# Performance work log

Hardware: AMD Instinct MI355X
Metric: run time of the kernel (lower is better)

## Reference

```python
import jax, jax.numpy as jnp
import numpy as np

N = 1_000_000
E = 1_000_000
K = 512
H = 64
F_IN = 19
N_ITERS = 3
EPS = 1e-5

def _leaky(x):
    return jax.nn.leaky_relu(x, negative_slope=0.01)

def _layernorm(x, g, b):
    mu = jnp.mean(x, axis=-1, keepdims=True)
    var = jnp.var(x, axis=-1, keepdims=True)
    return (x - mu) * jax.lax.rsqrt(var + EPS) * g + b

def setup_inputs() -> dict:
    key = jax.random.key(0)
    ks = jax.random.split(key, 20)
    s = 0.1
    inp = {
        "x": jax.random.normal(ks[0], (N, F_IN), dtype=jnp.float32),
        "edge_index": jax.random.randint(ks[1], (2, E), 0, N, dtype=jnp.int64),
        "candidate_indices": jax.random.randint(ks[2], (K,), 0, N, dtype=jnp.int64),
        # embedding params
        "pW_in": jax.random.normal(ks[3], (F_IN, H), dtype=jnp.float32) * s,
        "pb_in": jnp.zeros((H,), dtype=jnp.float32),
        "eW": jax.random.normal(ks[4], (2, H, H), dtype=jnp.float32) * s,
        "eb": jnp.zeros((2, H), dtype=jnp.float32),
        "gamma": jnp.ones((2, H), dtype=jnp.float32),
        "beta": jnp.zeros((2, H), dtype=jnp.float32),
        # bottom-up step MLPs (stacked over n_iters)
        "sW1": jax.random.normal(ks[5], (N_ITERS, H, H), dtype=jnp.float32) * s,
        "sb1": jnp.zeros((N_ITERS, H), dtype=jnp.float32),
        "sW2": jax.random.normal(ks[6], (N_ITERS, H, H), dtype=jnp.float32) * s,
        "sb2": jnp.zeros((N_ITERS, H), dtype=jnp.float32),
        # score head
        "hW1": jax.random.normal(ks[7], (H, H), dtype=jnp.float32) * s,
        "hb1": jnp.zeros((H,), dtype=jnp.float32),
        "hW2": jax.random.normal(ks[8], (H, 1), dtype=jnp.float32) * s,
        "hb2": jnp.zeros((1,), dtype=jnp.float32),
    }
    return inp

def reference(x, edge_index, candidate_indices, pW_in, pb_in, eW, eb, gamma, beta,
              sW1, sb1, sW2, sb2, hW1, hb1, hW2, hb2):
    # TreeNodeEmbedding: proj + 2 residual layers with LayerNorm
    h = _leaky(x @ pW_in + pb_in)
    for i in range(2):
        h = _layernorm(h + _leaky(h @ eW[i] + eb[i]), gamma[i], beta[i])
    parent_idx = edge_index[0]
    child_idx = edge_index[1]
    # Bottom-up message passing: scatter-mean over children, tiny MLP update
    for i in range(N_ITERS):
        child_h = h[child_idx]                                   # [E, H] gather
        sum_p = jax.ops.segment_sum(child_h, parent_idx, num_segments=N)  # [N, H]
        cnt = jax.ops.segment_sum(jnp.ones((E,), dtype=h.dtype), parent_idx, num_segments=N)  # [N]
        mean_p = sum_p / jnp.maximum(cnt, 1.0)[:, None]
        mask = (cnt > 0)[:, None]
        delta = _leaky(mean_p @ sW1[i] + sb1[i]) @ sW2[i] + sb2[i]
        h = h + jnp.where(mask, delta, 0.0)
    # Score head on candidates, softmax over k (all candidates real -> full_logits == scores)
    cand_h = h[candidate_indices]                                # [K, H]
    scores = (_leaky(cand_h @ hW1 + hb1) @ hW2 + hb2)[:, 0]      # [K]
    probs = jax.nn.softmax(scores)
    return probs
```

## Files before the change

### kernel.cpp

```cpp
#include <hip/hip_runtime.h>
#include <hip/hip_bf16.h>
#include <math.h>

#define H 64
#define FIN 19
#define EPSLN 1e-5f

#define TB 1024
#define NWV 16
#define NBLK 256

#define OFF_PW   0
#define OFF_PB   1280
#define OFF_EW   1344
#define OFF_EB   9536
#define OFF_G    9664
#define OFF_BT   9792
#define OFF_W1   9920
#define OFF_W2   22208
#define OFF_B1   34496
#define OFF_B2   34688
#define OFF_HW1  34880
#define OFF_HB1  38976
#define OFF_HW2  39040
#define OFF_HB2  39104
#define WTS_TOTAL 39105

__device__ __forceinline__ float leaky(float v) { return v > 0.f ? v : 0.01f * v; }

__device__ __forceinline__ float wsumf(float v) {
#pragma unroll
  for (int off = 32; off > 0; off >>= 1) v += __shfl_xor(v, off, 64);
  return v;
}

template <typename T>
__device__ __forceinline__ void cst(T* p, T v) {
  __hip_atomic_store(p, v, __ATOMIC_RELAXED, __HIP_MEMORY_SCOPE_AGENT);
}
__device__ __forceinline__ int cld(const int* p) {
  return __hip_atomic_load(p, __ATOMIC_RELAXED, __HIP_MEMORY_SCOPE_AGENT);
}

__device__ __forceinline__ void wsync() {
  asm volatile("" ::: "memory");
  __builtin_amdgcn_wave_barrier();
  asm volatile("" ::: "memory");
}

__device__ __forceinline__ bool detect_bf16(const unsigned short* xs) {
  const int lane = threadIdx.x & 63;
  unsigned a = xs[lane], b = xs[64 + lane];
  unsigned ea = (a >> 7) & 0xFFu, ebx = (b >> 7) & 0xFFu;
  return !__any((int)(ea > 140u || ebx > 140u));
}

__device__ __forceinline__ bool detect_i64(const int* w) {
  const int lane = threadIdx.x & 63;
  return __all((int)(w[2 * lane + 1] == 0));
}

__device__ __forceinline__ float ldf(const void* p, size_t i, bool bf) {
  return bf ? __bfloat162float(((const __hip_bfloat16*)p)[i]) : ((const float*)p)[i];
}

struct WT {
  const void* src[14];
  int off[14], len[14], sl[14], rp[14], rs[14], cs[14];
};

__device__ __forceinline__ void prep_one(const WT& T, bool bf, float* wts, int i) {
  int p = 0;
  while (i >= T.off[p] + T.len[p]) ++p;
  const int loc = i - T.off[p];
  float v;
  if (T.rp[p] == 0) {
    v = ldf(T.src[p], loc, bf);
  } else {
    const int s = loc / T.sl[p];
    const int r = loc - s * T.sl[p];
    const int j = r / T.rp[p];
    const int k = r - j * T.rp[p];
    v = (k < T.rs[p])
            ? ldf(T.src[p], (size_t)s * T.rs[p] * T.cs[p] + (size_t)k * T.cs[p] + j, bf)
            : 0.f;
  }
  cst(&wts[i], v);
}

__global__ __launch_bounds__(256) void prep_wts(WT T, const unsigned short* xs,
                                                float* wts, int total) {
  const bool bf = detect_bf16(xs);
  for (int i = blockIdx.x * 256 + threadIdx.x; i < total; i += gridDim.x * 256)
    prep_one(T, bf, wts, i);
}

__device__ float embed_math(const void* x, const float* wts, float* stg, int v,
                            int lane, bool bf) {
  float xv = (lane < FIN) ? ldf(x, (size_t)v * FIN + lane, bf) : 0.f;
  wsync();
  stg[lane] = xv;
  wsync();
  const float* tp = wts + OFF_PW + lane * 20;
  float a0 = wts[OFF_PB + lane], a1 = 0.f, a2 = 0.f, a3 = 0.f;
#pragma unroll
  for (int k = 0; k < 20; k += 4) {
    float4 m = *(const float4*)&stg[k];
    float4 w = *(const float4*)&tp[k];
    a0 += m.x * w.x; a1 += m.y * w.y; a2 += m.z * w.z; a3 += m.w * w.w;
  }
  float h = leaky((a0 + a1) + (a2 + a3));
#pragma unroll
  for (int L = 0; L < 2; ++L) {
    wsync();
    stg[lane] = h;
    wsync();
    const float* tw = wts + OFF_EW + L * 4096 + lane * 64;
    a0 = wts[OFF_EB + L * 64 + lane]; a1 = a2 = a3 = 0.f;
#pragma unroll
    for (int k = 0; k < H; k += 4) {
      float4 m = *(const float4*)&stg[k];
      float4 w = *(const float4*)&tw[k];
      a0 += m.x * w.x; a1 += m.y * w.y; a2 += m.z * w.z; a3 += m.w * w.w;
    }
    float val = h + leaky((a0 + a1) + (a2 + a3));
    float mu = wsumf(val) * (1.f / 64.f);
    float d = val - mu;
    float var = wsumf(d * d) * (1.f / 64.f);
    h = d * (1.f / sqrtf(var + EPSLN)) * wts[OFF_G + L * 64 + lane] +
        wts[OFF_BT + L * 64 + lane];
  }
  return h;
}

__device__ float delta_math(const float* wts, float* stg, float mean, int it, int lane) {
  wsync();
  stg[lane] = mean;
  wsync();
  const float* w1 = wts + OFF_W1 + it * 4096 + lane * 64;
  float a0 = wts[OFF_B1 + it * 64 + lane], a1 = 0.f, a2 = 0.f, a3 = 0.f;
#pragma unroll
  for (int k = 0; k < H; k += 4) {
    float4 m = *(const float4*)&stg[k];
    float4 w = *(const float4*)&w1[k];
    a0 += m.x * w.x; a1 += m.y * w.y; a2 += m.z * w.z; a3 += m.w * w.w;
  }
  float t1 = leaky((a0 + a1) + (a2 + a3));
  wsync();
  stg[lane] = t1;
  wsync();
  const float* w2 = wts + OFF_W2 + it * 4096 + lane * 64;
  a0 = wts[OFF_B2 + it * 64 + lane]; a1 = a2 = a3 = 0.f;
#pragma unroll
  for (int k = 0; k < H; k += 4) {
    float4 m = *(const float4*)&stg[k];
    float4 w = *(const float4*)&w2[k];
    a0 += m.x * w.x; a1 += m.y * w.y; a2 += m.z * w.z; a3 += m.w * w.w;
  }
  wsync();
  return (a0 + a1) + (a2 + a3);
}

__device__ float score_math(const float* wts, float* stg, float hv, int lane) {
  wsync();
  stg[lane] = hv;
  wsync();
  const float* hw1 = wts + OFF_HW1 + lane * 64;
  float a0 = wts[OFF_HB1 + lane], a1 = 0.f, a2 = 0.f, a3 = 0.f;
#pragma unroll
  for (int k = 0; k < H; k += 4) {
    float4 m = *(const float4*)&stg[k];
    float4 w = *(const float4*)&hw1[k];
    a0 += m.x * w.x; a1 += m.y * w.y; a2 += m.z * w.z; a3 += m.w * w.w;
  }
  wsync();
  float t1 = leaky((a0 + a1) + (a2 + a3));
  return wsumf(t1 * wts[OFF_HW2 + lane]) + wts[OFF_HB2];
}

__global__ __launch_bounds__(256) void init_kernel(int* map, int nN, int* counters, int K,
                                                   int* ch3, int n3, int* ch2, int n2,
                                                   int* ch1, int n1) {
  const int tid = blockIdx.x * 256 + threadIdx.x;
  const int stride = gridDim.x * 256;
  for (int i = tid; i < nN; i += stride) map[i] = 0;
  for (int i = tid; i < n3; i += stride) ch3[i] = -1;
  for (int i = tid; i < n2; i += stride) ch2[i] = -1;
  for (int i = tid; i < n1; i += stride) ch1[i] = -1;
  if (tid < 3) counters[tid] = 0;
  if (tid == 3) counters[3] = K;
}

__global__ __launch_bounds__(64) void seed_kernel(const int* cand_raw, int K, int nN,
                                                  int* map, int* node3, int* nextSame3,
                                                  int* selfChild3, int* ctr2, int cap2,
                                                  int* node2) {
  const bool i64 = detect_i64(cand_raw);
  int t = blockIdx.x * 64 + threadIdx.x;
  if (t >= K) return;
  int cv = i64 ? cand_raw[2 * t] : cand_raw[t];
  unsigned n = (unsigned)cv;
  if (n >= (unsigned)nN) n = 0;
  node3[t] = (int)n;
  int enc = (1 << 24) | t;
  int old = atomicExch(&map[n], enc);
  nextSame3[t] = ((old >> 24) == 1) ? (old & 0xFFFFFF) : -1;
  int s = atomicAdd(ctr2, 1);
  if (s < cap2) { node2[s] = (int)n; selfChild3[t] = s; } else selfChild3[t] = 0;
}

__global__ __launch_bounds__(256) void regself_kernel(const int* ctrU_, int capU,
                                                      const int* nodeU, int* map, int epoch,
                                                      int* nextSameU, int* ctrD, int capD,
                                                      int* nodeD, int* selfChildU) {
  int cnt = *ctrU_; if (cnt > capU) cnt = capU;
  int t = blockIdx.x * 256 + threadIdx.x;
  if (t >= cnt) return;
  int n = nodeU[t];
  int enc = (epoch << 24) | t;
  int old = atomicExch(&map[n], enc);
  nextSameU[t] = ((old >> 24) == epoch) ? (old & 0xFFFFFF) : -1;
  int s = atomicAdd(ctrD, 1);
  if (s < capD) { nodeD[s] = n; selfChildU[t] = s; } else selfChildU[t] = 0;
}

__global__ __launch_bounds__(256) void scan_kernel(const int* eraw, int E, int nN,
                                                   const int* map, int epoch,
                                                   const int* nextSameU, int* childHeadU,
                                                   int* ctrD, int capD, int* nodeD,
                                                   int* childNextD) {
  const bool i64 = detect_i64(eraw);
  int e = blockIdx.x * 256 + threadIdx.x;
  if (e >= E) return;
  int pv = i64 ? eraw[2 * e] : eraw[e];
  unsigned p = (unsigned)pv;
  if (p >= (unsigned)nN) p = 0;
  int m = map[p];
  if ((m >> 24) != epoch) return;
  int cv = i64 ? eraw[2 * (E + e)] : eraw[E + e];
  unsigned c = (unsigned)cv;
  if (c >= (unsigned)nN) c = 0;
  int t = m & 0xFFFFFF;
  while (t >= 0) {
    int ct = atomicAdd(ctrD, 1);
    if (ct < capD) {
      nodeD[ct] = (int)c;
      childNextD[ct] = atomicExch(&childHeadU[t], ct);
    }
    t = nextSameU[t];
  }
}

__global__ __launch_bounds__(64) void eval0_kernel(const void* x, const int* ctr0_,
                                                   int cap0, const int* node0,
                                                   const float* wts, float* val0) {
  __shared__ float stg[H];
  int cnt = *ctr0_; if (cnt > cap0) cnt = cap0;
  const int t = blockIdx.x;
  if (t >= cnt) return;
  const int lane = threadIdx.x;
  const bool bf = detect_bf16((const unsigned short*)x);
  float h = embed_math(x, wts, stg, node0[t], lane, bf);
  val0[(size_t)t * H + lane] = h;
}

__global__ __launch_bounds__(64) void evalL_kernel(const int* ctrU_, int capU,
                                                   const int* selfChildU,
                                                   const int* childHeadU,
                                                   const int* childNextD,
                                                   const float* valD, float* valU,
                                                   const float* wts, int it) {
  __shared__ float stg[H];
  int cnt = *ctrU_; if (cnt > capU) cnt = capU;
  const int t = blockIdx.x;
  if (t >= cnt) return;
  const int lane = threadIdx.x;
  float hv = valD[(size_t)selfChildU[t] * H + lane];
  float acc = 0.f;
  int k = 0;
  int c = childHeadU[t];
  while (c >= 0) { acc += valD[(size_t)c * H + lane]; ++k; c = childNextD[c]; }
  if (k > 0) hv += delta_math(wts, stg, acc / (float)k, it, lane);
  valU[(size_t)t * H + lane] = hv;
}

__global__ __launch_bounds__(512) void score_kernel(
    const float* __restrict__ candH, const float* __restrict__ wts,
    const void* x, void* out, int K) {
  __shared__ float red[512];
  const int t = threadIdx.x;
  const bool bf = detect_bf16((const unsigned short*)x);
  float sc = 0.f;
  if (t < K) {
    float hr[H];
#pragma unroll
    for (int k = 0; k < H; k += 4) {
      float4 v = *(const float4*)&candH[(size_t)t * H + k];
      hr[k] = v.x; hr[k + 1] = v.y; hr[k + 2] = v.z; hr[k + 3] = v.w;
    }
    for (int j = 0; j < H; ++j) {
      float a = wts[OFF_HB1 + j];
#pragma unroll
      for (int k = 0; k < H; k += 4) {
        float4 w = *(const float4*)&wts[OFF_HW1 + j * 64 + k];
        a += hr[k] * w.x + hr[k + 1] * w.y + hr[k + 2] * w.z + hr[k + 3] * w.w;
      }
      sc += leaky(a) * wts[OFF_HW2 + j];
    }
    sc += wts[OFF_HB2];
  }
  red[t] = (t < K) ? sc : -3.0e38f;
  __syncthreads();
  for (int off = 256; off > 0; off >>= 1) {
    if (t < off) red[t] = fmaxf(red[t], red[t + off]);
    __syncthreads();
  }
  const float m = red[0];
  __syncthreads();
  const float ex = (t < K) ? expf(sc - m) : 0.f;
  red[t] = ex;
  __syncthreads();
  for (int off = 256; off > 0; off >>= 1) {
    if (t < off) red[t] += red[t + off];
    __syncthreads();
  }
  const float inv = 1.f / red[0];
  if (t < K) {
    float p = ex * inv;
    if (bf) ((__hip_bfloat16*)out)[t] = __float2bfloat16(p);
    else    ((float*)out)[t] = p;
  }
}

struct FA {
  const void* x; const void* edge; const void* cand; void* outp;
  int nN, E, K, CAP2, CAP1, CAP0;
  int *ctrl;
  int *map3, *map2, *map1;
  int *chHead3, *chHead2, *chHead1;
  float* wts;
  int *nextSame3, *selfCh3;
  int *nextSame2, *selfCh2, *chNext2;
  int *nextSame1, *selfCh1, *chNext1;
  int *node0, *chNext0;
  float *val0, *val1, *val2, *scores;
  WT T;
};

#define CLINE 32

__device__ __forceinline__ void gsync(int* ctrl, int& phase) {
  __syncthreads();
  if (threadIdx.x == 0) {
    ++phase;
    const int nB = (int)gridDim.x;
    const int clu = (int)blockIdx.x >> 5;
    const int nClu = (nB + 31) >> 5;
    int cluSize = nB - (clu << 5);
    if (cluSize > 32) cluSize = 32;
    asm volatile("" ::: "memory");
    int old = __hip_atomic_fetch_add(&ctrl[clu * CLINE], 1, __ATOMIC_RELAXED,
                                     __HIP_MEMORY_SCOPE_AGENT);
    if (old == phase * cluSize - 1) {
      int mold = __hip_atomic_fetch_add(&ctrl[64 * CLINE], 1, __ATOMIC_RELAXED,
                                        __HIP_MEMORY_SCOPE_AGENT);
      if (mold == phase * nClu - 1) {
#pragma unroll
        for (int f = 0; f < 32; ++f)
          __hip_atomic_store(&ctrl[(65 + f) * CLINE], phase, __ATOMIC_RELAXED,
                             __HIP_MEMORY_SCOPE_AGENT);
      }
    }
    int* myFlag = &ctrl[(65 + ((int)blockIdx.x & 31)) * CLINE];
    int guard = 0;
    while (__hip_atomic_load(myFlag, __ATOMIC_RELAXED,
                             __HIP_MEMORY_SCOPE_AGENT) < phase) {
      __builtin_amdgcn_s_sleep(2);
      if (++guard > (1 << 18)) break;
    }
    asm volatile("" ::: "memory");
  }
  __syncthreads();
}

__global__ __launch_bounds__(TB, 4) void fused_kernel(FA A) {
  __shared__ float smem[NWV * H];
  const int tid = threadIdx.x;
  const int lane = tid & 63;
  const int wib = tid >> 6;
  const int gtid = blockIdx.x * TB + tid;
  const int nthr = (int)gridDim.x * TB;
  const int waveId = blockIdx.x * NWV + wib;
  const int nWaves = (int)gridDim.x * NWV;
  float* stg = &smem[wib * H];
  int* ctrl = A.ctrl;
  int* c2 = &ctrl[97 * CLINE];
  int* c1 = &ctrl[98 * CLINE];
  int* c0 = &ctrl[99 * CLINE];
  int phase = 0;

  const bool bf = detect_bf16((const unsigned short*)A.x);
  const int* eraw = (const int*)A.edge;
  const int* craw = (const int*)A.cand;
  const bool i64e = detect_i64(eraw);
  const bool i64c = detect_i64(craw);

  for (int i = gtid; i < WTS_TOTAL; i += nthr) prep_one(A.T, bf, A.wts, i);
  for (int t = gtid; t < A.K; t += nthr) {
    int cv = i64c ? craw[2 * t] : craw[t];
    unsigned n = (unsigned)cv;
    if (n >= (unsigned)A.nN) n = 0;
    cst(&A.nextSame3[t], atomicExch(&A.map3[(int)n], t));
    int s = atomicAdd(c2, 1);
    if (s < A.CAP2) {
      cst(&A.selfCh3[t], s);
      cst(&A.nextSame2[s], atomicExch(&A.map2[(int)n], s));
      int s1 = atomicAdd(c1, 1);
      if (s1 < A.CAP1) {
        cst(&A.selfCh2[s], s1);
        cst(&A.nextSame1[s1], atomicExch(&A.map1[(int)n], s1));
        int s0 = atomicAdd(c0, 1);
        if (s0 < A.CAP0) { cst(&A.node0[s0], (int)n); cst(&A.selfCh1[s1], s0); }
        else cst(&A.selfCh1[s1], 0);
      } else cst(&A.selfCh2[s], 0);
    } else cst(&A.selfCh3[t], 0);
  }
  gsync(ctrl, phase);

  for (int e = gtid; e < A.E; e += nthr) {
    int pv = i64e ? eraw[2 * e] : eraw[e];
    unsigned p = (unsigned)pv;
    if (p >= (unsigned)A.nN) p = 0;
    int t = A.map3[p];
    if (t < 0) continue;
    int cv = i64e ? eraw[2 * (A.E + e)] : eraw[A.E + e];
    unsigned cn = (unsigned)cv;
    if (cn >= (unsigned)A.nN) cn = 0;
    for (; t >= 0; t = A.nextSame3[t]) {
      int ct = atomicAdd(c2, 1);
      if (ct < A.CAP2) {
        cst(&A.chNext2[ct], atomicExch(&A.chHead3[t], ct));
        cst(&A.nextSame2[ct], atomicExch(&A.map2[(int)cn], ct));
        int s1 = atomicAdd(c1, 1);
        if (s1 < A.CAP1) {
          cst(&A.selfCh2[ct], s1);
          cst(&A.nextSame1[s1], atomicExch(&A.map1[(int)cn], s1));
          int s0 = atomicAdd(c0, 1);
          if (s0 < A.CAP0) { cst(&A.node0[s0], (int)cn); cst(&A.selfCh1[s1], s0); }
          else cst(&A.selfCh1[s1], 0);
        } else cst(&A.selfCh2[ct], 0);
      }
    }
  }
  gsync(ctrl, phase);

  for (int e = gtid; e < A.E; e += nthr) {
    int pv = i64e ? eraw[2 * e] : eraw[e];
    unsigned p = (unsigned)pv;
    if (p >= (unsigned)A.nN) p = 0;
    int t = A.map2[p];
    if (t < 0) continue;
    int cv = i64e ? eraw[2 * (A.E + e)] : eraw[A.E + e];
    unsigned cn = (unsigned)cv;
    if (cn >= (unsigned)A.nN) cn = 0;
    for (; t >= 0; t = A.nextSame2[t]) {
      int ct = atomicAdd(c1, 1);
      if (ct < A.CAP1) {
        cst(&A.chNext1[ct], atomicExch(&A.chHead2[t], ct));
        cst(&A.nextSame1[ct], atomicExch(&A.map1[(int)cn], ct));
        int s0 = atomicAdd(c0, 1);
        if (s0 < A.CAP0) { cst(&A.node0[s0], (int)cn); cst(&A.selfCh1[ct], s0); }
        else cst(&A.selfCh1[ct], 0);
      }
    }
  }
  gsync(ctrl, phase);

  for (int e = gtid; e < A.E; e += nthr) {
    int pv = i64e ? eraw[2 * e] : eraw[e];
    unsigned p = (unsigned)pv;
    if (p >= (unsigned)A.nN) p = 0;
    int t = A.map1[p];
    if (t < 0) continue;
    int cv = i64e ? eraw[2 * (A.E + e)] : eraw[A.E + e];
    unsigned cn = (unsigned)cv;
    if (cn >= (unsigned)A.nN) cn = 0;
    for (; t >= 0; t = A.nextSame1[t]) {
      int ct = atomicAdd(c0, 1);
      if (ct < A.CAP0) {
        cst(&A.node0[ct], (int)cn);
        cst(&A.chNext0[ct], atomicExch(&A.chHead1[t], ct));
      }
    }
  }
  gsync(ctrl, phase);

  {
    int cnt = cld(c0);
    if (cnt > A.CAP0) cnt = A.CAP0;
    for (int t = waveId; t < cnt; t += nWaves) {
      float h = embed_math(A.x, A.wts, stg, A.node0[t], lane, bf);
      cst(&A.val0[(size_t)t * H + lane], h);
    }
  }
  gsync(ctrl, phase);

  {
    int cnt = cld(c1);
    if (cnt > A.CAP1) cnt = A.CAP1;
    for (int t = waveId; t < cnt; t += nWaves) {
      float hv = A.val0[(size_t)A.selfCh1[t] * H + lane];
      float acc = 0.f;
      int kc = 0;
      for (int c = A.chHead1[t]; c >= 0; c = A.chNext0[c]) {
        acc += A.val0[(size_t)c * H + lane];
        ++kc;
      }
      if (kc > 0) hv += delta_math(A.wts, stg, acc / (float)kc, 0, lane);
      cst(&A.val1[(size_t)t * H + lane], hv);
    }
  }
  gsync(ctrl, phase);

  {
    int cnt = cld(c2);
    if (cnt > A.CAP2) cnt = A.CAP2;
    for (int t = waveId; t < cnt; t += nWaves) {
      float hv = A.val1[(size_t)A.selfCh2[t] * H + lane];
      float acc = 0.f;
      int kc = 0;
      for (int c = A.chHead2[t]; c >= 0; c = A.chNext1[c]) {
        acc += A.val1[(size_t)c * H + lane];
        ++kc;
      }
      if (kc > 0) hv += delta_math(A.wts, stg, acc / (float)kc, 1, lane);
      cst(&A.val2[(size_t)t * H + lane], hv);
    }
  }
  gsync(ctrl, phase);

  for (int t = waveId; t < A.K; t += nWaves) {
    float hv = A.val2[(size_t)A.selfCh3[t] * H + lane];
    float acc = 0.f;
    int kc = 0;
    for (int c = A.chHead3[t]; c >= 0; c = A.chNext2[c]) {
      acc += A.val2[(size_t)c * H + lane];
      ++kc;
    }
    if (kc > 0) hv += delta_math(A.wts, stg, acc / (float)kc, 2, lane);
    float sc = score_math(A.wts, stg, hv, lane);
    if (lane == 0) cst(&A.scores[t], sc);
  }
  gsync(ctrl, phase);

  if (blockIdx.x == 0) {
    __shared__ float red[TB];
    float lm = -3.0e38f;
    for (int i = tid; i < A.K; i += TB) lm = fmaxf(lm, A.scores[i]);
    red[tid] = lm;
    __syncthreads();
    for (int off = TB / 2; off > 0; off >>= 1) {
      if (tid < off) red[tid] = fmaxf(red[tid], red[tid + off]);
      __syncthreads();
    }
    const float m = red[0];
    __syncthreads();
    float ls = 0.f;
    for (int i = tid; i < A.K; i += TB) {
      float e = expf(A.scores[i] - m);
      A.scores[i] = e;
      ls += e;
    }
    red[tid] = ls;
    __syncthreads();
    for (int off = TB / 2; off > 0; off >>= 1) {
      if (tid < off) red[tid] += red[tid + off];
      __syncthreads();
    }
    const float inv = 1.f / red[0];
    for (int i = tid; i < A.K; i += TB) {
      float pv = A.scores[i] * inv;
      if (bf) ((__hip_bfloat16*)A.outp)[i] = __float2bfloat16(pv);
      else    ((float*)A.outp)[i] = pv;
    }
  }
}

extern "C" void kernel_launch(void* const* d_in, const int* in_sizes, int n_in,
                              void* d_out, int out_size, void* d_ws, size_t ws_size,
                              hipStream_t stream) {
  const void* x   = d_in[0];
  const int* edge = (const int*)d_in[1];
  const int* cand = (const int*)d_in[2];
  const int nN = in_sizes[0] / FIN;
  const int E  = in_sizes[1] / 2;
  const int K  = in_sizes[2];

  if (K > 2048 || K < 128 || E < 128 || nN < 1) return;

  const int CAP2 = 8 * K, CAP1 = 16 * K, CAP0 = 32 * K;

  auto al = [](size_t b) -> size_t { return (b + 255) & ~(size_t)255; };
  const size_t szW   = (size_t)WTS_TOTAL * sizeof(float);
  const size_t szMap = (size_t)nN * sizeof(int);
  const size_t szK   = (size_t)K * sizeof(int);
  const size_t sz2   = (size_t)CAP2 * sizeof(int);
  const size_t sz1   = (size_t)CAP1 * sizeof(int);
  const size_t sz0   = (size_t)CAP0 * sizeof(int);
  const size_t szV0  = (size_t)CAP0 * H * sizeof(float);
  const size_t szV1  = (size_t)CAP1 * H * sizeof(float);
  const size_t szV2  = (size_t)CAP2 * H * sizeof(float);
  const size_t szV3  = (size_t)K * H * sizeof(float);
  const size_t szCtrl = 16384;

  WT T;
  auto setv = [&](int i, const void* s, int o, int l) {
    T.src[i] = s; T.off[i] = o; T.len[i] = l; T.sl[i] = l;
    T.rp[i] = 0; T.rs[i] = 0; T.cs[i] = 0;
  };
  auto setm = [&](int i, const void* s, int o, int l, int sl, int rpad, int rs, int cs) {
    T.src[i] = s; T.off[i] = o; T.len[i] = l; T.sl[i] = sl;
    T.rp[i] = rpad; T.rs[i] = rs; T.cs[i] = cs;
  };
  setm(0,  d_in[3],  OFF_PW,  1280, 1280, 20, 19, 64);
  setv(1,  d_in[4],  OFF_PB,  64);
  setm(2,  d_in[5],  OFF_EW,  8192, 4096, 64, 64, 64);
  setv(3,  d_in[6],  OFF_EB,  128);
  setv(4,  d_in[7],  OFF_G,   128);
  setv(5,  d_in[8],  OFF_BT,  128);
  setm(6,  d_in[9],  OFF_W1,  12288, 4096, 64, 64, 64);
  setm(7,  d_in[11], OFF_W2,  12288, 4096, 64, 64, 64);
  setv(8,  d_in[10], OFF_B1,  192);
  setv(9,  d_in[12], OFF_B2,  192);
  setm(10, d_in[13], OFF_HW1, 4096, 4096, 64, 64, 64);
  setv(11, d_in[14], OFF_HB1, 64);
  setv(12, d_in[15], OFF_HW2, 64);
  setv(13, d_in[16], OFF_HB2, 1);

  int dev = 0, nCU = 0, maxB = 0;
  bool okq = (hipGetDevice(&dev) == hipSuccess) &&
             (hipDeviceGetAttribute(&nCU, hipDeviceAttributeMultiprocessorCount,
                                    dev) == hipSuccess) &&
             (hipOccupancyMaxActiveBlocksPerMultiprocessor(&maxB, fused_kernel, TB,
                                                           0) == hipSuccess) &&
             nCU >= 8 && maxB >= 1;

  const size_t needF = al(szCtrl) + 3 * al(szMap) + al(szK) + al(sz2) + al(sz1) +
                       al(szW) + 2 * al(szK) + 3 * al(sz2) + 3 * al(sz1) +
                       2 * al(sz0) + al(szV0) + al(szV1) + al(szV2) + al(szK);

  if (okq && ws_size >= needF) {
    char* wsb = (char*)d_ws;
    size_t off = 0;
    auto carve = [&](size_t bytes) -> void* {
      void* p = wsb + off;
      off += (bytes + 255) & ~(size_t)255;
      return p;
    };
    FA A;
    A.x = x; A.edge = edge; A.cand = cand; A.outp = d_out;
    A.nN = nN; A.E = E; A.K = K; A.CAP2 = CAP2; A.CAP1 = CAP1; A.CAP0 = CAP0;
    A.ctrl = (int*)carve(szCtrl);
    char* ffs = wsb + off;
    A.map3 = (int*)carve(szMap);
    A.map2 = (int*)carve(szMap);
    A.map1 = (int*)carve(szMap);
    A.chHead3 = (int*)carve(szK);
    A.chHead2 = (int*)carve(sz2);
    A.chHead1 = (int*)carve(sz1);
    const size_t ffbytes = (size_t)((wsb + off) - ffs);
    A.wts = (float*)carve(szW);
    A.nextSame3 = (int*)carve(szK); A.selfCh3 = (int*)carve(szK);
    A.nextSame2 = (int*)carve(sz2); A.selfCh2 = (int*)carve(sz2);
    A.chNext2 = (int*)carve(sz2);
    A.nextSame1 = (int*)carve(sz1); A.selfCh1 = (int*)carve(sz1);
    A.chNext1 = (int*)carve(sz1);
    A.node0 = (int*)carve(sz0); A.chNext0 = (int*)carve(sz0);
    A.val0 = (float*)carve(szV0); A.val1 = (float*)carve(szV1);
    A.val2 = (float*)carve(szV2);
    A.scores = (float*)carve(szK);
    A.T = T;

    int g = NBLK;
    if (g > nCU * maxB) g = nCU * maxB;
    if (g > 2048) g = 2048;
    if (g >= 8) {
      hipMemsetAsync(A.ctrl, 0, szCtrl, stream);
      hipMemsetAsync(ffs, 0xFF, ffbytes, stream);
      fused_kernel<<<g, TB, 0, stream>>>(A);
      return;
    }
  }

  {
    const size_t need = al(szW) + al(szMap) + 256 +
                        4 * al(szK) + 5 * al(sz2) + 5 * al(sz1) + 2 * al(sz0) +
                        al(szV0) + al(szV1) + al(szV2) + al(szV3);
    if (ws_size < need) return;

    char* wsb = (char*)d_ws;
    size_t off = 0;
    auto carve = [&](size_t bytes) -> void* {
      void* p = wsb + off;
      off += (bytes + 255) & ~(size_t)255;
      return p;
    };
    float* wts     = (float*)carve(szW);
    int* map       = (int*)carve(szMap);
    int* counters  = (int*)carve(256);
    int* node3     = (int*)carve(szK);
    int* nextSame3 = (int*)carve(szK);
    int* selfCh3   = (int*)carve(szK);
    int* chHead3   = (int*)carve(szK);
    int* node2     = (int*)carve(sz2);
    int* nextSame2 = (int*)carve(sz2);
    int* selfCh2   = (int*)carve(sz2);
    int* chHead2   = (int*)carve(sz2);
    int* chNext2   = (int*)carve(sz2);
    int* node1     = (int*)carve(sz1);
    int* nextSame1 = (int*)carve(sz1);
    int* selfCh1   = (int*)carve(sz1);
    int* chHead1   = (int*)carve(sz1);
    int* chNext1   = (int*)carve(sz1);
    int* node0     = (int*)carve(sz0);
    int* chNext0   = (int*)carve(sz0);
    float* val0    = (float*)carve(szV0);
    float* val1    = (float*)carve(szV1);
    float* val2    = (float*)carve(szV2);
    float* val3    = (float*)carve(szV3);

    prep_wts<<<160, 256, 0, stream>>>(T, (const unsigned short*)x, wts, WTS_TOTAL);
    init_kernel<<<1024, 256, 0, stream>>>(map, nN, counters, K, chHead3, K,
                                          chHead2, CAP2, chHead1, CAP1);
    seed_kernel<<<(K + 63) / 64, 64, 0, stream>>>(cand, K, nN, map, node3, nextSame3,
                                                  selfCh3, &counters[0], CAP2, node2);
    scan_kernel<<<(E + 255) / 256, 256, 0, stream>>>(edge, E, nN, map, 1, nextSame3,
                                                     chHead3, &counters[0], CAP2,
                                                     node2, chNext2);
    regself_kernel<<<(CAP2 + 255) / 256, 256, 0, stream>>>(&counters[0], CAP2, node2, map, 2,
                                                           nextSame2, &counters[1], CAP1,
                                                           node1, selfCh2);
    scan_kernel<<<(E + 255) / 256, 256, 0, stream>>>(edge, E, nN, map, 2, nextSame2,
                                                     chHead2, &counters[1], CAP1,
                                                     node1, chNext1);
    regself_kernel<<<(CAP1 + 255) / 256, 256, 0, stream>>>(&counters[1], CAP1, node1, map, 3,
                                                           nextSame1, &counters[2], CAP0,
                                                           node0, selfCh1);
    scan_kernel<<<(E + 255) / 256, 256, 0, stream>>>(edge, E, nN, map, 3, nextSame1,
                                                     chHead1, &counters[2], CAP0,
                                                     node0, chNext0);

    eval0_kernel<<<CAP0, 64, 0, stream>>>(x, &counters[2], CAP0, node0, wts, val0);
    evalL_kernel<<<CAP1, 64, 0, stream>>>(&counters[1], CAP1, selfCh1, chHead1, chNext0,
                                          val0, val1, wts, 0);
    evalL_kernel<<<CAP2, 64, 0, stream>>>(&counters[0], CAP2, selfCh2, chHead2, chNext1,
                                          val1, val2, wts, 1);
    evalL_kernel<<<K, 64, 0, stream>>>(&counters[3], K, selfCh3, chHead3, chNext2,
                                       val2, val3, wts, 2);

    score_kernel<<<1, 512, 0, stream>>>(val3, wts, x, d_out, K);
  }
}
```

Baseline: 269.1 us.

## Replace dense node maps with hashed open-addressing tables and unified slot layout

Swaps the three dense per-node maps (sized by N and memset to 0xFF each call) for small open-addressing hash tables keyed by node id, so the setup memset shrinks to a single small zero fill. Slot indices are unified across levels so a node's own embedding slot doubles as its child slot, which removes the selfCh indirection arrays and extra atomics. The grid is also doubled to 512 blocks. The cost is CAS-based probing on every registration and probing on every edge lookup in place of a direct array read.

```diff
diff --git a/kernel.cpp b/kernel.cpp
--- a/kernel.cpp
+++ b/kernel.cpp
@@ -8,7 +8,7 @@
 
 #define TB 1024
 #define NWV 16
-#define NBLK 256
+#define NBLK 512
 
 #define OFF_PW   0
 #define OFF_PB   1280
@@ -34,12 +34,20 @@
   return v;
 }
 
+__device__ __forceinline__ int imin(int a, int b) { return a < b ? a : b; }
+
 template <typename T>
 __device__ __forceinline__ void cst(T* p, T v) {
   __hip_atomic_store(p, v, __ATOMIC_RELAXED, __HIP_MEMORY_SCOPE_AGENT);
 }
 __device__ __forceinline__ int cld(const int* p) {
   return __hip_atomic_load(p, __ATOMIC_RELAXED, __HIP_MEMORY_SCOPE_AGENT);
+}
+__device__ __forceinline__ int axc(int* p, int v) {
+  return __hip_atomic_exchange(p, v, __ATOMIC_RELAXED, __HIP_MEMORY_SCOPE_AGENT);
+}
+__device__ __forceinline__ int afa(int* p, int v) {
+  return __hip_atomic_fetch_add(p, v, __ATOMIC_RELAXED, __HIP_MEMORY_SCOPE_AGENT);
 }
 
 __device__ __forceinline__ void wsync() {
@@ -176,6 +184,40 @@
   wsync();
   float t1 = leaky((a0 + a1) + (a2 + a3));
   return wsumf(t1 * wts[OFF_HW2 + lane]) + wts[OFF_HB2];
+}
+
+__device__ __forceinline__ void reg(int* keys, int* vals, unsigned mask, int n,
+                                    int id, int* nextSame) {
+  unsigned h = (((unsigned)n * 2654435761u) >> 10) & mask;
+  for (unsigned probe = 0; probe <= mask; ++probe) {
+    int expected = 0;
+    int k;
+    if (__hip_atomic_compare_exchange_strong(&keys[h], &expected, n + 1,
+                                             __ATOMIC_RELAXED, __ATOMIC_RELAXED,
+                                             __HIP_MEMORY_SCOPE_AGENT))
+      k = n + 1;
+    else
+      k = expected;
+    if (k == n + 1) {
+      int old = axc(&vals[h], id + 1);
+      cst(&nextSame[id], old);
+      return;
+    }
+    h = (h + 1) & mask;
+  }
+  cst(&nextSame[id], 0);
+}
+
+__device__ __forceinline__ int lookup(const int* keys, const int* vals,
+                                      unsigned mask, int n) {
+  unsigned h = (((unsigned)n * 2654435761u) >> 10) & mask;
+  for (unsigned probe = 0; probe <= mask; ++probe) {
+    int k = keys[h];
+    if (k == 0) return 0;
+    if (k == n + 1) return vals[h];
+    h = (h + 1) & mask;
+  }
+  return 0;
 }
 
 __global__ __launch_bounds__(256) void init_kernel(int* map, int nN, int* counters, int K,
@@ -336,13 +378,14 @@
   const void* x; const void* edge; const void* cand; void* outp;
   int nN, E, K, CAP2, CAP1, CAP0;
   int *ctrl;
-  int *map3, *map2, *map1;
+  int *t3k, *t2k, *t1k;
   int *chHead3, *chHead2, *chHead1;
+  unsigned m3, m2, m1;
+  int *t3v, *t2v, *t1v;
   float* wts;
-  int *nextSame3, *selfCh3;
-  int *nextSame2, *selfCh2, *chNext2;
-  int *nextSame1, *selfCh1, *chNext1;
-  int *node0, *chNext0;
+  int *nextSame3, *nextSame2, *nextSame1;
+  int *chNext2, *chNext1, *chNext0;
+  int *node0;
   float *val0, *val1, *val2, *scores;
   WT T;
 };
@@ -359,22 +402,18 @@
     int cluSize = nB - (clu << 5);
     if (cluSize > 32) cluSize = 32;
     asm volatile("" ::: "memory");
-    int old = __hip_atomic_fetch_add(&ctrl[clu * CLINE], 1, __ATOMIC_RELAXED,
-                                     __HIP_MEMORY_SCOPE_AGENT);
+    int old = afa(&ctrl[clu * CLINE], 1);
     if (old == phase * cluSize - 1) {
-      int mold = __hip_atomic_fetch_add(&ctrl[64 * CLINE], 1, __ATOMIC_RELAXED,
-                                        __HIP_MEMORY_SCOPE_AGENT);
+      int mold = afa(&ctrl[64 * CLINE], 1);
       if (mold == phase * nClu - 1) {
 #pragma unroll
         for (int f = 0; f < 32; ++f)
-          __hip_atomic_store(&ctrl[(65 + f) * CLINE], phase, __ATOMIC_RELAXED,
-                             __HIP_MEMORY_SCOPE_AGENT);
+          cst(&ctrl[(65 + f) * CLINE], phase);
       }
     }
     int* myFlag = &ctrl[(65 + ((int)blockIdx.x & 31)) * CLINE];
     int guard = 0;
-    while (__hip_atomic_load(myFlag, __ATOMIC_RELAXED,
-                             __HIP_MEMORY_SCOPE_AGENT) < phase) {
+    while (cld(myFlag) < phase) {
       __builtin_amdgcn_s_sleep(2);
       if (++guard > (1 << 18)) break;
     }
@@ -394,9 +433,9 @@
   const int nWaves = (int)gridDim.x * NWV;
   float* stg = &smem[wib * H];
   int* ctrl = A.ctrl;
-  int* c2 = &ctrl[97 * CLINE];
-  int* c1 = &ctrl[98 * CLINE];
-  int* c0 = &ctrl[99 * CLINE];
+  int* n2 = &ctrl[97 * CLINE];
+  int* n1 = &ctrl[98 * CLINE];
+  int* n0 = &ctrl[99 * CLINE];
   int phase = 0;
 
   const bool bf = detect_bf16((const unsigned short*)A.x);
@@ -410,20 +449,10 @@
     int cv = i64c ? craw[2 * t] : craw[t];
     unsigned n = (unsigned)cv;
     if (n >= (unsigned)A.nN) n = 0;
-    cst(&A.nextSame3[t], atomicExch(&A.map3[(int)n], t));
-    int s = atomicAdd(c2, 1);
-    if (s < A.CAP2) {
-      cst(&A.selfCh3[t], s);
-      cst(&A.nextSame2[s], atomicExch(&A.map2[(int)n], s));
-      int s1 = atomicAdd(c1, 1);
-      if (s1 < A.CAP1) {
-        cst(&A.selfCh2[s], s1);
-        cst(&A.nextSame1[s1], atomicExch(&A.map1[(int)n], s1));
-        int s0 = atomicAdd(c0, 1);
-        if (s0 < A.CAP0) { cst(&A.node0[s0], (int)n); cst(&A.selfCh1[s1], s0); }
-        else cst(&A.selfCh1[s1], 0);
-      } else cst(&A.selfCh2[s], 0);
-    } else cst(&A.selfCh3[t], 0);
+    cst(&A.node0[t], (int)n);
+    reg(A.t3k, A.t3v, A.m3, (int)n, t, A.nextSame3);
+    reg(A.t2k, A.t2v, A.m2, (int)n, t, A.nextSame2);
+    reg(A.t1k, A.t1v, A.m1, (int)n, t, A.nextSame1);
   }
   gsync(ctrl, phase);
 
@@ -431,24 +460,19 @@
     int pv = i64e ? eraw[2 * e] : eraw[e];
     unsigned p = (unsigned)pv;
     if (p >= (unsigned)A.nN) p = 0;
-    int t = A.map3[p];
-    if (t < 0) continue;
+    int head = lookup(A.t3k, A.t3v, A.m3, (int)p);
+    if (head == 0) continue;
     int cv = i64e ? eraw[2 * (A.E + e)] : eraw[A.E + e];
     unsigned cn = (unsigned)cv;
     if (cn >= (unsigned)A.nN) cn = 0;
-    for (; t >= 0; t = A.nextSame3[t]) {
-      int ct = atomicAdd(c2, 1);
+    for (int tp = head; tp > 0; tp = A.nextSame3[tp - 1]) {
+      int t = tp - 1;
+      int ct = A.K + afa(n2, 1);
       if (ct < A.CAP2) {
-        cst(&A.chNext2[ct], atomicExch(&A.chHead3[t], ct));
-        cst(&A.nextSame2[ct], atomicExch(&A.map2[(int)cn], ct));
-        int s1 = atomicAdd(c1, 1);
-        if (s1 < A.CAP1) {
-          cst(&A.selfCh2[ct], s1);
-          cst(&A.nextSame1[s1], atomicExch(&A.map1[(int)cn], s1));
-          int s0 = atomicAdd(c0, 1);
-          if (s0 < A.CAP0) { cst(&A.node0[s0], (int)cn); cst(&A.selfCh1[s1], s0); }
-          else cst(&A.selfCh1[s1], 0);
-        } else cst(&A.selfCh2[ct], 0);
+        cst(&A.node0[ct], (int)cn);
+        cst(&A.chNext2[ct], axc(&A.chHead3[t], ct + 1));
+        reg(A.t2k, A.t2v, A.m2, (int)cn, ct, A.nextSame2);
+        reg(A.t1k, A.t1v, A.m1, (int)cn, ct, A.nextSame1);
       }
     }
   }
@@ -458,19 +482,18 @@
     int pv = i64e ? eraw[2 * e] : eraw[e];
     unsigned p = (unsigned)pv;
     if (p >= (unsigned)A.nN) p = 0;
-    int t = A.map2[p];
-    if (t < 0) continue;
+    int head = lookup(A.t2k, A.t2v, A.m2, (int)p);
+    if (head == 0) continue;
     int cv = i64e ? eraw[2 * (A.E + e)] : eraw[A.E + e];
     unsigned cn = (unsigned)cv;
     if (cn >= (unsigned)A.nN) cn = 0;
-    for (; t >= 0; t = A.nextSame2[t]) {
-      int ct = atomicAdd(c1, 1);
+    for (int sp = head; sp > 0; sp = A.nextSame2[sp - 1]) {
+      int s = sp - 1;
+      int ct = A.CAP2 + afa(n1, 1);
       if (ct < A.CAP1) {
-        cst(&A.chNext1[ct], atomicExch(&A.chHead2[t], ct));
-        cst(&A.nextSame1[ct], atomicExch(&A.map1[(int)cn], ct));
-        int s0 = atomicAdd(c0, 1);
-        if (s0 < A.CAP0) { cst(&A.node0[s0], (int)cn); cst(&A.selfCh1[ct], s0); }
-        else cst(&A.selfCh1[ct], 0);
+        cst(&A.node0[ct], (int)cn);
+        cst(&A.chNext1[ct], axc(&A.chHead2[s], ct + 1));
+        reg(A.t1k, A.t1v, A.m1, (int)cn, ct, A.nextSame1);
       }
     }
   }
@@ -480,71 +503,74 @@
     int pv = i64e ? eraw[2 * e] : eraw[e];
     unsigned p = (unsigned)pv;
     if (p >= (unsigned)A.nN) p = 0;
-    int t = A.map1[p];
-    if (t < 0) continue;
+    int head = lookup(A.t1k, A.t1v, A.m1, (int)p);
+    if (head == 0) continue;
     int cv = i64e ? eraw[2 * (A.E + e)] : eraw[A.E + e];
     unsigned cn = (unsigned)cv;
     if (cn >= (unsigned)A.nN) cn = 0;
-    for (; t >= 0; t = A.nextSame1[t]) {
-      int ct = atomicAdd(c0, 1);
+    for (int sp = head; sp > 0; sp = A.nextSame1[sp - 1]) {
+      int s = sp - 1;
+      int ct = A.CAP1 + afa(n0, 1);
       if (ct < A.CAP0) {
         cst(&A.node0[ct], (int)cn);
-        cst(&A.chNext0[ct], atomicExch(&A.chHead1[t], ct));
+        cst(&A.chNext0[ct], axc(&A.chHead1[s], ct + 1));
       }
     }
   }
   gsync(ctrl, phase);
 
+  const int cnt2 = A.K + imin(cld(n2), A.CAP2 - A.K);
+  const int cc1  = imin(cld(n1), A.CAP1 - A.CAP2);
+  const int cc0  = imin(cld(n0), A.CAP0 - A.CAP1);
+
   {
-    int cnt = cld(c0);
-    if (cnt > A.CAP0) cnt = A.CAP0;
-    for (int t = waveId; t < cnt; t += nWaves) {
-      float h = embed_math(A.x, A.wts, stg, A.node0[t], lane, bf);
-      cst(&A.val0[(size_t)t * H + lane], h);
+    const int total0 = cnt2 + cc1 + cc0;
+    for (int i = waveId; i < total0; i += nWaves) {
+      int slot = i < cnt2 ? i
+               : (i < cnt2 + cc1 ? A.CAP2 + (i - cnt2)
+                                 : A.CAP1 + (i - cnt2 - cc1));
+      float h = embed_math(A.x, A.wts, stg, A.node0[slot], lane, bf);
+      cst(&A.val0[(size_t)slot * H + lane], h);
     }
   }
   gsync(ctrl, phase);
 
   {
-    int cnt = cld(c1);
-    if (cnt > A.CAP1) cnt = A.CAP1;
-    for (int t = waveId; t < cnt; t += nWaves) {
-      float hv = A.val0[(size_t)A.selfCh1[t] * H + lane];
+    const int total1 = cnt2 + cc1;
+    for (int i = waveId; i < total1; i += nWaves) {
+      int s = i < cnt2 ? i : A.CAP2 + (i - cnt2);
+      float hv = A.val0[(size_t)s * H + lane];
       float acc = 0.f;
       int kc = 0;
-      for (int c = A.chHead1[t]; c >= 0; c = A.chNext0[c]) {
-        acc += A.val0[(size_t)c * H + lane];
+      for (int cp = A.chHead1[s]; cp > 0; cp = A.chNext0[cp - 1]) {
+        acc += A.val0[(size_t)(cp - 1) * H + lane];
         ++kc;
       }
       if (kc > 0) hv += delta_math(A.wts, stg, acc / (float)kc, 0, lane);
-      cst(&A.val1[(size_t)t * H + lane], hv);
+      cst(&A.val1[(size_t)s * H + lane], hv);
     }
   }
   gsync(ctrl, phase);
 
-  {
-    int cnt = cld(c2);
-    if (cnt > A.CAP2) cnt = A.CAP2;
-    for (int t = waveId; t < cnt; t += nWaves) {
-      float hv = A.val1[(size_t)A.selfCh2[t] * H + lane];
-      float acc = 0.f;
-      int kc = 0;
-      for (int c = A.chHead2[t]; c >= 0; c = A.chNext1[c]) {
-        acc += A.val1[(size_t)c * H + lane];
-        ++kc;
-      }
-      if (kc > 0) hv += delta_math(A.wts, stg, acc / (float)kc, 1, lane);
-      cst(&A.val2[(size_t)t * H + lane], hv);
-    }
-  }
-  gsync(ctrl, phase);
-
-  for (int t = waveId; t < A.K; t += nWaves) {
-    float hv = A.val2[(size_t)A.selfCh3[t] * H + lane];
+  for (int s = waveId; s < cnt2; s += nWaves) {
+    float hv = A.val1[(size_t)s * H + lane];
     float acc = 0.f;
     int kc = 0;
-    for (int c = A.chHead3[t]; c >= 0; c = A.chNext2[c]) {
-      acc += A.val2[(size_t)c * H + lane];
+    for (int cp = A.chHead2[s]; cp > 0; cp = A.chNext1[cp - 1]) {
+      acc += A.val1[(size_t)(cp - 1) * H + lane];
+      ++kc;
+    }
+    if (kc > 0) hv += delta_math(A.wts, stg, acc / (float)kc, 1, lane);
+    cst(&A.val2[(size_t)s * H + lane], hv);
+  }
+  gsync(ctrl, phase);
+
+  for (int t = waveId; t < A.K; t += nWaves) {
+    float hv = A.val2[(size_t)t * H + lane];
+    float acc = 0.f;
+    int kc = 0;
+    for (int cp = A.chHead3[t]; cp > 0; cp = A.chNext2[cp - 1]) {
+      acc += A.val2[(size_t)(cp - 1) * H + lane];
       ++kc;
     }
     if (kc > 0) hv += delta_math(A.wts, stg, acc / (float)kc, 2, lane);
@@ -601,6 +627,7 @@
   const int CAP2 = 8 * K, CAP1 = 16 * K, CAP0 = 32 * K;
 
   auto al = [](size_t b) -> size_t { return (b + 255) & ~(size_t)255; };
+  auto np2 = [](int x) -> int { int p = 8; while (p < x) p <<= 1; return p; };
   const size_t szW   = (size_t)WTS_TOTAL * sizeof(float);
   const size_t szMap = (size_t)nN * sizeof(int);
   const size_t szK   = (size_t)K * sizeof(int);
@@ -612,6 +639,9 @@
   const size_t szV2  = (size_t)CAP2 * H * sizeof(float);
   const size_t szV3  = (size_t)K * H * sizeof(float);
   const size_t szCtrl = 16384;
+
+  const int t3s = np2(K) * 4, t2s = np2(CAP2) * 4, t1s = np2(CAP1) * 4;
+  const size_t szT3 = (size_t)t3s * 4, szT2 = (size_t)t2s * 4, szT1 = (size_t)t1s * 4;
 
   WT T;
   auto setv = [&](int i, const void* s, int o, int l) {
@@ -645,9 +675,13 @@
                                                            0) == hipSuccess) &&
              nCU >= 8 && maxB >= 1;
 
-  const size_t needF = al(szCtrl) + 3 * al(szMap) + al(szK) + al(sz2) + al(sz1) +
-                       al(szW) + 2 * al(szK) + 3 * al(sz2) + 3 * al(sz1) +
-                       2 * al(sz0) + al(szV0) + al(szV1) + al(szV2) + al(szK);
+  const size_t needF = al(szCtrl) + al(szT3) + al(szT2) + al(szT1) +
+                       al(szK) + al(sz2) + al(sz1) +
+                       al(szT3) + al(szT2) + al(szT1) +
+                       al(szW) + al(szK) + al(sz2) + al(sz1) +
+                       al(sz2) + al(sz1) + al(sz0) +
+                       al(sz0) +
+                       al(szV0) + al(szV1) + al(szV2) + al(szK);
 
   if (okq && ws_size >= needF) {
     char* wsb = (char*)d_ws;
@@ -660,23 +694,28 @@
     FA A;
     A.x = x; A.edge = edge; A.cand = cand; A.outp = d_out;
     A.nN = nN; A.E = E; A.K = K; A.CAP2 = CAP2; A.CAP1 = CAP1; A.CAP0 = CAP0;
+    A.m3 = (unsigned)(t3s - 1); A.m2 = (unsigned)(t2s - 1); A.m1 = (unsigned)(t1s - 1);
     A.ctrl = (int*)carve(szCtrl);
-    char* ffs = wsb + off;
-    A.map3 = (int*)carve(szMap);
-    A.map2 = (int*)carve(szMap);
-    A.map1 = (int*)carve(szMap);
+    A.t3k = (int*)carve(szT3);
+    A.t2k = (int*)carve(szT2);
+    A.t1k = (int*)carve(szT1);
     A.chHead3 = (int*)carve(szK);
     A.chHead2 = (int*)carve(sz2);
     A.chHead1 = (int*)carve(sz1);
-    const size_t ffbytes = (size_t)((wsb + off) - ffs);
+    const size_t zbytes = off;
+    A.t3v = (int*)carve(szT3);
+    A.t2v = (int*)carve(szT2);
+    A.t1v = (int*)carve(szT1);
     A.wts = (float*)carve(szW);
-    A.nextSame3 = (int*)carve(szK); A.selfCh3 = (int*)carve(szK);
-    A.nextSame2 = (int*)carve(sz2); A.selfCh2 = (int*)carve(sz2);
+    A.nextSame3 = (int*)carve(szK);
+    A.nextSame2 = (int*)carve(sz2);
+    A.nextSame1 = (int*)carve(sz1);
     A.chNext2 = (int*)carve(sz2);
-    A.nextSame1 = (int*)carve(sz1); A.selfCh1 = (int*)carve(sz1);
     A.chNext1 = (int*)carve(sz1);
-    A.node0 = (int*)carve(sz0); A.chNext0 = (int*)carve(sz0);
-    A.val0 = (float*)carve(szV0); A.val1 = (float*)carve(szV1);
+    A.chNext0 = (int*)carve(sz0);
+    A.node0 = (int*)carve(sz0);
+    A.val0 = (float*)carve(szV0);
+    A.val1 = (float*)carve(szV1);
     A.val2 = (float*)carve(szV2);
     A.scores = (float*)carve(szK);
     A.T = T;
@@ -685,8 +724,7 @@
     if (g > nCU * maxB) g = nCU * maxB;
     if (g > 2048) g = 2048;
     if (g >= 8) {
-      hipMemsetAsync(A.ctrl, 0, szCtrl, stream);
-      hipMemsetAsync(ffs, 0xFF, ffbytes, stream);
+      hipMemsetAsync(d_ws, 0, zbytes, stream);
       fused_kernel<<<g, TB, 0, stream>>>(A);
       return;
     }
```

Result: no change. 273.1 us (+1.5%).
